# Performance work log

Hardware: AMD Instinct MI355X
Metric: run time of the kernel (lower is better)

The kernel has to match this reference:

```python
import jax, jax.numpy as jnp
import numpy as np

N_NODES = 50000
IN_CH = 512
OUT_CH = 512
N_EDGES = 800000


def setup_inputs() -> dict:
    key = jax.random.key(0)
    k_x, k_e, k_w, k_b = jax.random.split(key, 4)
    x = jax.random.normal(k_x, (N_NODES, IN_CH), dtype=jnp.float32)
    edge_index = jax.random.randint(k_e, (2, N_EDGES), 0, N_NODES, dtype=jnp.int32)
    # nn.Linear(in_channels*2, out_channels): weight (out, 2*in), bias (out,)
    bound = 1.0 / np.sqrt(2 * IN_CH)
    W = jax.random.uniform(k_w, (OUT_CH, 2 * IN_CH), minval=-bound, maxval=bound, dtype=jnp.float32)
    b = jax.random.uniform(k_b, (OUT_CH,), minval=-bound, maxval=bound, dtype=jnp.float32)
    return {"x": x, "edge_index": edge_index, "W": W, "b": b}


def reference(x, edge_index, W, b):
    # SAGE(v) = W . concat(h_v, mean_{u in N(v)} h_u) + b
    src, dst = edge_index[0], edge_index[1]
    src_feats = x[src]                                        # (E, C) gather
    neighbor_sum = jax.ops.segment_sum(src_feats, dst, num_segments=x.shape[0])  # (N, C)
    neighbor_count = jax.ops.segment_sum(
        jnp.ones((src.shape[0],), dtype=x.dtype), dst, num_segments=x.shape[0]
    )                                                          # (N,)
    neighbor_count = jnp.maximum(neighbor_count, 1.0)
    neighbor_mean = neighbor_sum / neighbor_count[:, None]
    h = jnp.concatenate([x, neighbor_mean], axis=-1)           # (N, 2C)
    return h @ W.T + b                                         # (N, out)
```

## Files before the change

### kernel.cpp

```cpp
#include <hip/hip_runtime.h>
#include <stdint.h>

#define CI 512
#define CO 512
#define CPAD 8

typedef __attribute__((ext_vector_type(4))) float f32x4;
typedef __attribute__((ext_vector_type(8))) __bf16 bf16x8;

#define AS1 __attribute__((address_space(1)))
#define AS3 __attribute__((address_space(3)))

__device__ __forceinline__ unsigned short f2bf_bits(float f) {
  union { float f; unsigned int u; } v; v.f = f;
  unsigned int u = v.u;
  unsigned int lsb = (u >> 16) & 1u;
  u += 0x7fffu + lsb;
  return (unsigned short)(u >> 16);
}

__global__ void k_prep(const float* __restrict__ x, unsigned short* __restrict__ xb, int nx4,
                       const float* __restrict__ W, unsigned short* __restrict__ Wb, int nw4,
                       const int* __restrict__ dst, int* __restrict__ cnt, int E,
                       int bx, int bw) {
  const int b = blockIdx.x;
  if (b < bx) {
    int i = b * 256 + threadIdx.x;
    if (i < nx4) {
      float4 v = reinterpret_cast<const float4*>(x)[i];
      ushort4 o;
      o.x = f2bf_bits(v.x); o.y = f2bf_bits(v.y);
      o.z = f2bf_bits(v.z); o.w = f2bf_bits(v.w);
      reinterpret_cast<ushort4*>(xb)[i] = o;
    }
  } else if (b < bx + bw) {
    int i = (b - bx) * 256 + threadIdx.x;
    if (i < nw4) {
      float4 v = reinterpret_cast<const float4*>(W)[i];
      ushort4 o;
      o.x = f2bf_bits(v.x); o.y = f2bf_bits(v.y);
      o.z = f2bf_bits(v.z); o.w = f2bf_bits(v.w);
      reinterpret_cast<ushort4*>(Wb)[i] = o;
    }
  } else {
    int e = (b - bx - bw) * 256 + threadIdx.x;
    if (e < E) atomicAdd(&cnt[dst[e] * CPAD], 1);
  }
}

__global__ void k_bsum(const int* __restrict__ cnt, int* __restrict__ bsum, int n) {
  int t = threadIdx.x;
  int i = blockIdx.x * 256 + t;
  int v = (i < n) ? cnt[(size_t)i * CPAD] : 0;
  #pragma unroll
  for (int off = 32; off; off >>= 1) v += __shfl_down(v, off, 64);
  __shared__ int ws[4];
  if ((t & 63) == 0) ws[t >> 6] = v;
  __syncthreads();
  if (t == 0) bsum[blockIdx.x] = ws[0] + ws[1] + ws[2] + ws[3];
}

__global__ void k_scanf(const int* __restrict__ cnt, const int* __restrict__ bsum,
                        int* __restrict__ rowptr, int n, int nb) {
  int t = threadIdx.x, lane = t & 63, w = t >> 6;
  __shared__ int ws1[4], ws2[4], sboff;

  int v0 = (t < nb) ? bsum[t] : 0;
  int s0 = v0;
  #pragma unroll
  for (int off = 1; off < 64; off <<= 1) {
    int u = __shfl_up(s0, off, 64);
    if (lane >= off) s0 += u;
  }
  if (lane == 63) ws1[w] = s0;
  __syncthreads();
  if (t == blockIdx.x) {
    int add0 = 0;
    for (int j = 0; j < w; ++j) add0 += ws1[j];
    sboff = s0 + add0 - v0;
  }
  __syncthreads();

  int i = blockIdx.x * 256 + t;
  int v = (i < n) ? cnt[(size_t)i * CPAD] : 0;
  int s = v;
  #pragma unroll
  for (int off = 1; off < 64; off <<= 1) {
    int u = __shfl_up(s, off, 64);
    if (lane >= off) s += u;
  }
  if (lane == 63) ws2[w] = s;
  __syncthreads();
  int add = sboff;
  for (int j = 0; j < w; ++j) add += ws2[j];
  if (i < n) rowptr[i + 1] = s + add;
  if (i == 0) rowptr[0] = 0;
}

__global__ void k_fill(const int* __restrict__ src, const int* __restrict__ dst,
                       const int* __restrict__ rowptr, int* __restrict__ cursor,
                       unsigned short* __restrict__ csr, int E) {
  int e = blockIdx.x * 256 + threadIdx.x;
  if (e < E) {
    int d = dst[e];
    int pos = atomicAdd(&cursor[(size_t)d * CPAD], 1);
    csr[rowptr[d] + pos] = (unsigned short)src[e];
  }
}

__device__ __forceinline__ void acc8(float* s, uint4 r) {
  const unsigned int u[4] = {r.x, r.y, r.z, r.w};
  #pragma unroll
  for (int k = 0; k < 4; ++k) {
    union { unsigned int u; float f; } lo, hi;
    lo.u = u[k] << 16;
    hi.u = u[k] & 0xffff0000u;
    s[2 * k]     += lo.f;
    s[2 * k + 1] += hi.f;
  }
}

__global__ __launch_bounds__(256) void k_aggregate(
    const unsigned short* __restrict__ xb,
    const int* __restrict__ rowptr,
    const unsigned short* __restrict__ csr,
    unsigned short* __restrict__ meanS, int Nn) {
  const int s  = blockIdx.x & 7;
  const int nb = blockIdx.x >> 3;
  const int wv = threadIdx.x >> 6;
  const int lane = threadIdx.x & 63;
  const int g = lane >> 3, li = lane & 7;
  const int node = nb * 32 + wv * 8 + g;

  int beg = 0, deg = 0;
  if (node < Nn) {
    beg = rowptr[node];
    deg = rowptr[node + 1] - beg;
  }
  float acc[8] = {};
  const unsigned short* __restrict__ xs = xb + s * 64 + li * 8;

  int j = 0;
  for (; j + 2 <= deg; j += 2) {
    int i0 = (int)csr[beg + j];
    int i1 = (int)csr[beg + j + 1];
    uint4 r0 = *reinterpret_cast<const uint4*>(xs + (size_t)i0 * CI);
    uint4 r1 = *reinterpret_cast<const uint4*>(xs + (size_t)i1 * CI);
    acc8(acc, r0);
    acc8(acc, r1);
  }
  if (j < deg) {
    int i0 = (int)csr[beg + j];
    uint4 r0 = *reinterpret_cast<const uint4*>(xs + (size_t)i0 * CI);
    acc8(acc, r0);
  }

  if (node < Nn) {
    const float inv = 1.f / fmaxf((float)deg, 1.f);
    unsigned short ob[8];
    #pragma unroll
    for (int k = 0; k < 8; ++k) ob[k] = f2bf_bits(acc[k] * inv);
    uint4 w;
    w.x = (unsigned int)ob[0] | ((unsigned int)ob[1] << 16);
    w.y = (unsigned int)ob[2] | ((unsigned int)ob[3] << 16);
    w.z = (unsigned int)ob[4] | ((unsigned int)ob[5] << 16);
    w.w = (unsigned int)ob[6] | ((unsigned int)ob[7] << 16);
    *reinterpret_cast<uint4*>(meanS + ((size_t)s * Nn + node) * 64 + li * 8) = w;
  }
}

#define BM 256
#define BN 128
#define BK 64
#define SLOT_SH 24576
#define BOFF 16384
#define EPAD 132

#define WAITV(N) asm volatile("s_waitcnt vmcnt(" #N ")" ::: "memory")

__global__ __launch_bounds__(512) void k_gemm(
    const unsigned short* __restrict__ xb,
    const unsigned short* __restrict__ meanS,
    const unsigned short* __restrict__ Wb,
    const float* __restrict__ bias,
    float* __restrict__ out, int M) {
  __shared__ unsigned short lds[3 * SLOT_SH];
  const int tid = threadIdx.x;

  const int wg = (blockIdx.x & 7) * 98 + (blockIdx.x >> 3);
  const int tm = wg >> 2, tn = wg & 3;
  const int m0 = tm * BM, n0 = tn * BN;
  const int lane = tid & 63, wvid = tid >> 6;
  const int wm = wvid >> 2, wn = wvid & 3;
  const int lrow = lane & 15;

  int gra[4], asrc8[4];
  #pragma unroll
  for (int i = 0; i < 4; ++i) {
    int idx = i * 512 + tid;
    int r = idx >> 3;
    asrc8[i] = ((idx & 7) ^ (r & 7)) * 8;
    int g = m0 + r;
    gra[i] = g < M ? g : M - 1;
  }
  int brow[2], bsrc8[2];
  #pragma unroll
  for (int i = 0; i < 2; ++i) {
    int idx = i * 512 + tid;
    int r = idx >> 3;
    brow[i] = r;
    bsrc8[i] = ((idx & 7) ^ (r & 7)) * 8;
  }

  const size_t Nn64 = (size_t)M * 64;

  f32x4 acc[8][2] = {};

  auto stage = [&](int kt, int sl) {
    unsigned short* sa = &lds[sl * SLOT_SH];
    unsigned short* sb = sa + BOFF;
    if (kt < 8) {
      const int ka = kt * 64;
      #pragma unroll
      for (int i = 0; i < 4; ++i)
        __builtin_amdgcn_global_load_lds(
          (const AS1 unsigned int*)(uintptr_t)(xb + (size_t)gra[i] * CI + ka + asrc8[i]),
          (AS3 unsigned int*)(uintptr_t)(&sa[(size_t)(i * 512 + tid) * 8]), 16, 0, 0);
    } else {
      const unsigned short* __restrict__ A = meanS + (size_t)(kt - 8) * Nn64;
      #pragma unroll
      for (int i = 0; i < 4; ++i)
        __builtin_amdgcn_global_load_lds(
          (const AS1 unsigned int*)(uintptr_t)(A + (size_t)gra[i] * 64 + asrc8[i]),
          (AS3 unsigned int*)(uintptr_t)(&sa[(size_t)(i * 512 + tid) * 8]), 16, 0, 0);
    }
    const int kw = kt * 64;
    #pragma unroll
    for (int i = 0; i < 2; ++i)
      __builtin_amdgcn_global_load_lds(
        (const AS1 unsigned int*)(uintptr_t)(Wb + (size_t)(n0 + brow[i]) * (2 * CI) + kw + bsrc8[i]),
        (AS3 unsigned int*)(uintptr_t)(&sb[(size_t)(i * 512 + tid) * 8]), 16, 0, 0);
  };

  auto compute = [&](int sl) {
    const unsigned short* __restrict__ La = &lds[sl * SLOT_SH];
    const unsigned short* __restrict__ Lb = La + BOFF;
    #pragma unroll
    for (int kk = 0; kk < 2; ++kk) {
      const int crd = kk * 4 + (lane >> 4);
      bf16x8 af[8], bf[2];
      #pragma unroll
      for (int mi = 0; mi < 8; ++mi) {
        const int rr = wm * 128 + mi * 16 + lrow;
        af[mi] = *reinterpret_cast<const bf16x8*>(&La[rr * BK + ((crd ^ (rr & 7)) * 8)]);
      }
      #pragma unroll
      for (int ni = 0; ni < 2; ++ni) {
        const int rb = wn * 32 + ni * 16 + lrow;
        bf[ni] = *reinterpret_cast<const bf16x8*>(&Lb[rb * BK + ((crd ^ (rb & 7)) * 8)]);
      }
      __builtin_amdgcn_s_setprio(1);
      #pragma unroll
      for (int mi = 0; mi < 8; ++mi)
        #pragma unroll
        for (int ni = 0; ni < 2; ++ni)
          acc[mi][ni] = __builtin_amdgcn_mfma_f32_16x16x32_bf16(af[mi], bf[ni], acc[mi][ni], 0, 0, 0);
      __builtin_amdgcn_s_setprio(0);
    }
  };

  stage(0, 0);
  stage(1, 1);

  #pragma unroll
  for (int t = 0; t < 16; ++t) {
    if (t < 14) {
      stage(t + 2, (t + 2) % 3);
      WAITV(12);
    } else if (t == 14) {
      WAITV(6);
    } else {
      WAITV(0);
    }
    __builtin_amdgcn_s_barrier();
    __builtin_amdgcn_sched_barrier(0);
    compute(t % 3);
    __builtin_amdgcn_sched_barrier(0);
    __builtin_amdgcn_s_barrier();
  }

  __syncthreads();
  float* ldsf = reinterpret_cast<float*>(&lds[0]);
  const int lj = lane >> 4;
  float bv[2];
  #pragma unroll
  for (int ni = 0; ni < 2; ++ni) bv[ni] = bias[n0 + wn * 32 + ni * 16 + lrow];

  #pragma unroll
  for (int c = 0; c < 8; ++c) {
    if (wm == (c >> 2)) {
      #pragma unroll
      for (int mi2 = 0; mi2 < 2; ++mi2) {
        const int mi = (c & 3) * 2 + mi2;
        #pragma unroll
        for (int ni = 0; ni < 2; ++ni)
          #pragma unroll
          for (int j = 0; j < 4; ++j)
            ldsf[(mi2 * 16 + lj * 4 + j) * EPAD + wn * 32 + ni * 16 + lrow] = acc[mi][ni][j] + bv[ni];
      }
    }
    __syncthreads();
    #pragma unroll
    for (int p = 0; p < 2; ++p) {
      int linear = p * 512 + tid;
      int rl = linear >> 5;
      int c4 = (linear & 31) << 2;
      int row = m0 + c * 32 + rl;
      if (row < M) {
        float4 v = *reinterpret_cast<const float4*>(&ldsf[rl * EPAD + c4]);
        *reinterpret_cast<float4*>(&out[(size_t)row * CO + n0 + c4]) = v;
      }
    }
    __syncthreads();
  }
}

extern "C" void kernel_launch(void* const* d_in, const int* in_sizes, int n_in,
                              void* d_out, int out_size, void* d_ws, size_t ws_size,
                              hipStream_t stream) {
  (void)n_in; (void)out_size; (void)ws_size;
  const float* x    = (const float*)d_in[0];
  const int*   ei   = (const int*)d_in[1];
  const float* W    = (const float*)d_in[2];
  const float* bias = (const float*)d_in[3];
  float* out = (float*)d_out;

  const int Nn = in_sizes[0] / CI;
  const int E  = in_sizes[1] / 2;
  const int* src = ei;
  const int* dst = ei + E;

  const int nblk = (Nn + 255) / 256;

  int* cnt    = (int*)d_ws;
  int* cursor = cnt + (size_t)Nn * CPAD;
  int* rowptr = cursor + (size_t)Nn * CPAD;
  int* bsum   = rowptr + (Nn + 1);
  uintptr_t p = (uintptr_t)(bsum + nblk);
  p = (p + 255) & ~(uintptr_t)255;
  unsigned short* csr = (unsigned short*)p;
  p = (uintptr_t)(csr + E);
  p = (p + 255) & ~(uintptr_t)255;
  unsigned short* xb    = (unsigned short*)p;
  unsigned short* meanS = xb + (size_t)Nn * CI;
  unsigned short* Wb    = meanS + (size_t)Nn * CI;

  hipMemsetAsync(cnt, 0, (size_t)2 * Nn * CPAD * sizeof(int), stream);

  const int nx4 = (Nn * CI) / 4;
  const int nw4 = (CO * 2 * CI) / 4;
  const int bx = (nx4 + 255) / 256;
  const int bw = (nw4 + 255) / 256;
  const int be = (E + 255) / 256;
  k_prep<<<bx + bw + be, 256, 0, stream>>>(x, xb, nx4, W, Wb, nw4, dst, cnt, E, bx, bw);
  k_bsum<<<nblk, 256, 0, stream>>>(cnt, bsum, Nn);
  k_scanf<<<nblk, 256, 0, stream>>>(cnt, bsum, rowptr, Nn, nblk);
  k_fill<<<(E + 255) / 256, 256, 0, stream>>>(src, dst, rowptr, cursor, csr, E);

  const int nab = ((Nn + 31) / 32) * 8;
  k_aggregate<<<nab, 256, 0, stream>>>(xb, rowptr, csr, meanS, Nn);

  const int mtiles = (Nn + BM - 1) / BM;
  k_gemm<<<mtiles * (CO / BN), 512, 0, stream>>>(xb, meanS, Wb, bias, out, Nn);
}
```

Baseline: 275.6 us.

## Shrink GEMM tile to 128x128 with 256 threads and double buffering

The GEMM block tile drops from 256x128 with 512 threads and a 3-stage LDS pipeline to 128x128 with 256 threads and 2 stages. The warp layout changes to 2x2 with 64x64 per warp, and the XCD-aware block remapping is generalised to any grid size. The intent is to use less LDS per block and raise occupancy, and the generalised remap also removes the hardcoded 98 in the old mapping. In exchange, the shallower pipeline hides load latency less well, and each output tile costs more redundant A/B traffic.

```diff
diff --git a/kernel.cpp b/kernel.cpp
--- a/kernel.cpp
+++ b/kernel.cpp
@@ -169,52 +169,50 @@
   }
 }
 
-#define BM 256
+#define BM 128
 #define BN 128
 #define BK 64
-#define SLOT_SH 24576
-#define BOFF 16384
+#define SLOT_SH 16384
+#define BOFF 8192
 #define EPAD 132
 
 #define WAITV(N) asm volatile("s_waitcnt vmcnt(" #N ")" ::: "memory")
 
-__global__ __launch_bounds__(512) void k_gemm(
+__global__ __launch_bounds__(256) void k_gemm(
     const unsigned short* __restrict__ xb,
     const unsigned short* __restrict__ meanS,
     const unsigned short* __restrict__ Wb,
     const float* __restrict__ bias,
     float* __restrict__ out, int M) {
-  __shared__ unsigned short lds[3 * SLOT_SH];
+  __shared__ unsigned short lds[2 * SLOT_SH];
   const int tid = threadIdx.x;
-
-  const int wg = (blockIdx.x & 7) * 98 + (blockIdx.x >> 3);
-  const int tm = wg >> 2, tn = wg & 3;
+  const int ntn = CO / BN;
+
+  const int nwg = gridDim.x;
+  const int q = nwg >> 3, r = nwg & 7;
+  const int xcd = blockIdx.x & 7, lid = blockIdx.x >> 3;
+  const int wg = (xcd < r ? xcd * (q + 1) : r * (q + 1) + (xcd - r) * q) + lid;
+
+  const int tm = wg / ntn, tn = wg % ntn;
   const int m0 = tm * BM, n0 = tn * BN;
   const int lane = tid & 63, wvid = tid >> 6;
-  const int wm = wvid >> 2, wn = wvid & 3;
+  const int wm = wvid >> 1, wn = wvid & 1;
   const int lrow = lane & 15;
 
-  int gra[4], asrc8[4];
+  int arow[4], gra[4], scol8[4];
   #pragma unroll
   for (int i = 0; i < 4; ++i) {
-    int idx = i * 512 + tid;
-    int r = idx >> 3;
-    asrc8[i] = ((idx & 7) ^ (r & 7)) * 8;
-    int g = m0 + r;
+    int idx = i * 256 + tid;
+    int rr = idx >> 3;
+    arow[i] = rr;
+    scol8[i] = ((idx & 7) ^ (rr & 7)) * 8;
+    int g = m0 + rr;
     gra[i] = g < M ? g : M - 1;
   }
-  int brow[2], bsrc8[2];
-  #pragma unroll
-  for (int i = 0; i < 2; ++i) {
-    int idx = i * 512 + tid;
-    int r = idx >> 3;
-    brow[i] = r;
-    bsrc8[i] = ((idx & 7) ^ (r & 7)) * 8;
-  }
 
   const size_t Nn64 = (size_t)M * 64;
 
-  f32x4 acc[8][2] = {};
+  f32x4 acc[4][4] = {};
 
   auto stage = [&](int kt, int sl) {
     unsigned short* sa = &lds[sl * SLOT_SH];
@@ -224,22 +222,22 @@
       #pragma unroll
       for (int i = 0; i < 4; ++i)
         __builtin_amdgcn_global_load_lds(
-          (const AS1 unsigned int*)(uintptr_t)(xb + (size_t)gra[i] * CI + ka + asrc8[i]),
-          (AS3 unsigned int*)(uintptr_t)(&sa[(size_t)(i * 512 + tid) * 8]), 16, 0, 0);
+          (const AS1 unsigned int*)(uintptr_t)(xb + (size_t)gra[i] * CI + ka + scol8[i]),
+          (AS3 unsigned int*)(uintptr_t)(&sa[(size_t)(i * 256 + tid) * 8]), 16, 0, 0);
     } else {
       const unsigned short* __restrict__ A = meanS + (size_t)(kt - 8) * Nn64;
       #pragma unroll
       for (int i = 0; i < 4; ++i)
         __builtin_amdgcn_global_load_lds(
-          (const AS1 unsigned int*)(uintptr_t)(A + (size_t)gra[i] * 64 + asrc8[i]),
-          (AS3 unsigned int*)(uintptr_t)(&sa[(size_t)(i * 512 + tid) * 8]), 16, 0, 0);
+          (const AS1 unsigned int*)(uintptr_t)(A + (size_t)gra[i] * 64 + scol8[i]),
+          (AS3 unsigned int*)(uintptr_t)(&sa[(size_t)(i * 256 + tid) * 8]), 16, 0, 0);
     }
     const int kw = kt * 64;
     #pragma unroll
-    for (int i = 0; i < 2; ++i)
+    for (int i = 0; i < 4; ++i)
       __builtin_amdgcn_global_load_lds(
-        (const AS1 unsigned int*)(uintptr_t)(Wb + (size_t)(n0 + brow[i]) * (2 * CI) + kw + bsrc8[i]),
-        (AS3 unsigned int*)(uintptr_t)(&sb[(size_t)(i * 512 + tid) * 8]), 16, 0, 0);
+        (const AS1 unsigned int*)(uintptr_t)(Wb + (size_t)(n0 + arow[i]) * (2 * CI) + kw + scol8[i]),
+        (AS3 unsigned int*)(uintptr_t)(&sb[(size_t)(i * 256 + tid) * 8]), 16, 0, 0);
   };
 
   auto compute = [&](int sl) {
@@ -248,80 +246,76 @@
     #pragma unroll
     for (int kk = 0; kk < 2; ++kk) {
       const int crd = kk * 4 + (lane >> 4);
-      bf16x8 af[8], bf[2];
-      #pragma unroll
-      for (int mi = 0; mi < 8; ++mi) {
-        const int rr = wm * 128 + mi * 16 + lrow;
+      bf16x8 af[4], bf[4];
+      #pragma unroll
+      for (int mi = 0; mi < 4; ++mi) {
+        const int rr = wm * 64 + mi * 16 + lrow;
         af[mi] = *reinterpret_cast<const bf16x8*>(&La[rr * BK + ((crd ^ (rr & 7)) * 8)]);
       }
       #pragma unroll
-      for (int ni = 0; ni < 2; ++ni) {
-        const int rb = wn * 32 + ni * 16 + lrow;
+      for (int ni = 0; ni < 4; ++ni) {
+        const int rb = wn * 64 + ni * 16 + lrow;
         bf[ni] = *reinterpret_cast<const bf16x8*>(&Lb[rb * BK + ((crd ^ (rb & 7)) * 8)]);
       }
       __builtin_amdgcn_s_setprio(1);
       #pragma unroll
-      for (int mi = 0; mi < 8; ++mi)
+      for (int mi = 0; mi < 4; ++mi)
         #pragma unroll
-        for (int ni = 0; ni < 2; ++ni)
+        for (int ni = 0; ni < 4; ++ni)
           acc[mi][ni] = __builtin_amdgcn_mfma_f32_16x16x32_bf16(af[mi], bf[ni], acc[mi][ni], 0, 0, 0);
       __builtin_amdgcn_s_setprio(0);
     }
   };
 
   stage(0, 0);
-  stage(1, 1);
 
   #pragma unroll
   for (int t = 0; t < 16; ++t) {
-    if (t < 14) {
-      stage(t + 2, (t + 2) % 3);
-      WAITV(12);
-    } else if (t == 14) {
-      WAITV(6);
+    if (t < 15) {
+      stage(t + 1, (t + 1) & 1);
+      WAITV(8);
     } else {
       WAITV(0);
     }
     __builtin_amdgcn_s_barrier();
     __builtin_amdgcn_sched_barrier(0);
-    compute(t % 3);
+    compute(t & 1);
     __builtin_amdgcn_sched_barrier(0);
     __builtin_amdgcn_s_barrier();
   }
 
   __syncthreads();
-  float* ldsf = reinterpret_cast<float*>(&lds[0]);
+  float* lds_c = reinterpret_cast<float*>(&lds[0]);
   const int lj = lane >> 4;
-  float bv[2];
-  #pragma unroll
-  for (int ni = 0; ni < 2; ++ni) bv[ni] = bias[n0 + wn * 32 + ni * 16 + lrow];
-
-  #pragma unroll
-  for (int c = 0; c < 8; ++c) {
-    if (wm == (c >> 2)) {
-      #pragma unroll
-      for (int mi2 = 0; mi2 < 2; ++mi2) {
-        const int mi = (c & 3) * 2 + mi2;
+  float bv[4];
+  #pragma unroll
+  for (int ni = 0; ni < 4; ++ni) bv[ni] = bias[n0 + wn * 64 + ni * 16 + lrow];
+
+  #pragma unroll
+  for (int cw = 0; cw < 2; ++cw) {
+    #pragma unroll
+    for (int mi = 0; mi < 4; ++mi) {
+      if (wm == cw) {
         #pragma unroll
-        for (int ni = 0; ni < 2; ++ni)
+        for (int ni = 0; ni < 4; ++ni)
           #pragma unroll
           for (int j = 0; j < 4; ++j)
-            ldsf[(mi2 * 16 + lj * 4 + j) * EPAD + wn * 32 + ni * 16 + lrow] = acc[mi][ni][j] + bv[ni];
+            lds_c[(lj * 4 + j) * EPAD + wn * 64 + ni * 16 + lrow] = acc[mi][ni][j] + bv[ni];
       }
-    }
-    __syncthreads();
-    #pragma unroll
-    for (int p = 0; p < 2; ++p) {
-      int linear = p * 512 + tid;
-      int rl = linear >> 5;
-      int c4 = (linear & 31) << 2;
-      int row = m0 + c * 32 + rl;
-      if (row < M) {
-        float4 v = *reinterpret_cast<const float4*>(&ldsf[rl * EPAD + c4]);
-        *reinterpret_cast<float4*>(&out[(size_t)row * CO + n0 + c4]) = v;
+      __syncthreads();
+      #pragma unroll
+      for (int p = 0; p < 2; ++p) {
+        int linear = p * 256 + tid;
+        int rl = linear >> 5;
+        int c4 = (linear & 31) << 2;
+        int row = m0 + cw * 64 + mi * 16 + rl;
+        if (row < M) {
+          float4 v = *reinterpret_cast<const float4*>(&lds_c[rl * EPAD + c4]);
+          *reinterpret_cast<float4*>(&out[(size_t)row * CO + n0 + c4]) = v;
+        }
       }
-    }
-    __syncthreads();
+      __syncthreads();
+    }
   }
 }
 
@@ -371,5 +365,5 @@
   k_aggregate<<<nab, 256, 0, stream>>>(xb, rowptr, csr, meanS, Nn);
 
   const int mtiles = (Nn + BM - 1) / BM;
-  k_gemm<<<mtiles * (CO / BN), 512, 0, stream>>>(xb, meanS, Wb, bias, out, Nn);
-}
+  k_gemm<<<mtiles * (CO / BN), 256, 0, stream>>>(xb, meanS, Wb, bias, out, Nn);
+}
```

Result: faster. 258.3 us (-6.3%).
